# Performance work log

Measured on AMD Instinct MI355X. Metric: run time of the kernel, lower is better.

Reference implementation:

```python
import jax, jax.numpy as jnp
import numpy as np

N = 16777216
BETA = 0.5  # SmoothL1Loss beta

def setup_inputs() -> dict:
    key = jax.random.key(0)
    k1, k2, k3 = jax.random.split(key, 3)
    outs = jax.random.normal(k1, (N,), dtype=jnp.float32)
    labels = jax.random.uniform(k2, (N,), dtype=jnp.float32)
    lens = jax.random.randint(k3, (N,), 1, 1000, dtype=jnp.int64)
    return {"outs": outs, "labels": labels, "lens": lens}

def reference(outs, labels, lens):
    d = outs - labels
    ad = jnp.abs(d)
    # per-element SmoothL1 (beta=0.5); single scalar reduces to 'mean' == value itself
    sl1 = jnp.where(ad < BETA, 0.5 * d * d / BETA, ad - 0.5 * BETA)
    # skip elements whose abs error is within 1/len boundary
    boundary = 1.0 / lens.astype(jnp.float32)
    mask = ad >= boundary
    total = jnp.sum(jnp.where(mask, sl1, 0.0))
    return total.reshape(1)
```

## Files before the change

kernel.cpp:

```cpp
#include <hip/hip_runtime.h>


#define N_TOTAL 16777216
#define NVEC    (N_TOTAL / 4)
#define UNROLL  4
#define BLOCK   256
#define GRID    (NVEC / (BLOCK * UNROLL))

__device__ __forceinline__ float sl1_term(float o, float l, int len) {
    float d  = o - l;
    float ad = fabsf(d);
    float v  = (ad < 0.5f) ? (d * d) : (ad - 0.25f);
    float boundary = 1.0f / (float)len;
    return (ad >= boundary) ? v : 0.0f;
}

__global__ __launch_bounds__(BLOCK) void RegressionLoss_45440753992375_kernel(
        const float* __restrict__ outs,
        const float* __restrict__ labels,
        const int*   __restrict__ lens,
        float* __restrict__ out) {
    const float4* o4 = (const float4*)outs;
    const float4* l4 = (const float4*)labels;
    const int4*   n4 = (const int4*)lens;

    const int base = blockIdx.x * (BLOCK * UNROLL) + threadIdx.x;

    float4 o[UNROLL], l[UNROLL];
    int4   ln[UNROLL];
    #pragma unroll
    for (int u = 0; u < UNROLL; ++u) o[u]  = o4[base + u * BLOCK];
    #pragma unroll
    for (int u = 0; u < UNROLL; ++u) l[u]  = l4[base + u * BLOCK];
    #pragma unroll
    for (int u = 0; u < UNROLL; ++u) ln[u] = n4[base + u * BLOCK];

    float acc = 0.0f;
    #pragma unroll
    for (int u = 0; u < UNROLL; ++u) {
        acc += sl1_term(o[u].x, l[u].x, ln[u].x);
        acc += sl1_term(o[u].y, l[u].y, ln[u].y);
        acc += sl1_term(o[u].z, l[u].z, ln[u].z);
        acc += sl1_term(o[u].w, l[u].w, ln[u].w);
    }

    #pragma unroll
    for (int off = 32; off > 0; off >>= 1)
        acc += __shfl_down(acc, off, 64);

    __shared__ float smem[BLOCK / 64];
    const int lane = threadIdx.x & 63;
    const int wid  = threadIdx.x >> 6;
    if (lane == 0) smem[wid] = acc;
    __syncthreads();
    if (threadIdx.x == 0) {
        float bsum = smem[0] + smem[1] + smem[2] + smem[3];
        atomicAdd(out, bsum);
    }
}

extern "C" void kernel_launch(void* const* d_in, const int* in_sizes, int n_in,
                              void* d_out, int out_size, void* d_ws, size_t ws_size,
                              hipStream_t stream) {
    const float* outs   = (const float*)d_in[0];
    const float* labels = (const float*)d_in[1];
    const int*   lens   = (const int*)d_in[2];
    float* out = (float*)d_out;

    hipMemsetAsync(out, 0, sizeof(float), stream);

    RegressionLoss_45440753992375_kernel<<<GRID, BLOCK, 0, stream>>>(outs, labels, lens, out);
}
```

Measured before the change: 201.0 us.

## Replace unrolled loads with grid-stride loop and one-deep register prefetch

Halves the grid and has each thread iterate over eight float4 chunks, issuing loads for the next chunk before computing the current one. The aim is to overlap memory latency with compute and reduce block count and atomics. It trades the previous four-way batched loads for a single-stage prefetch, which lowers the number of loads in flight per thread.

```diff
diff --git a/kernel.cpp b/kernel.cpp
--- a/kernel.cpp
+++ b/kernel.cpp
@@ -3,9 +3,9 @@
 
 #define N_TOTAL 16777216
 #define NVEC    (N_TOTAL / 4)
-#define UNROLL  4
 #define BLOCK   256
-#define GRID    (NVEC / (BLOCK * UNROLL))
+#define GRID    2048
+#define ITERS   (NVEC / (BLOCK * GRID))
 
 __device__ __forceinline__ float sl1_term(float o, float l, int len) {
     float d  = o - l;
@@ -24,25 +24,31 @@
     const float4* l4 = (const float4*)labels;
     const int4*   n4 = (const int4*)lens;
 
-    const int base = blockIdx.x * (BLOCK * UNROLL) + threadIdx.x;
+    int i = blockIdx.x * (BLOCK * ITERS) + threadIdx.x;
 
-    float4 o[UNROLL], l[UNROLL];
-    int4   ln[UNROLL];
-    #pragma unroll
-    for (int u = 0; u < UNROLL; ++u) o[u]  = o4[base + u * BLOCK];
-    #pragma unroll
-    for (int u = 0; u < UNROLL; ++u) l[u]  = l4[base + u * BLOCK];
-    #pragma unroll
-    for (int u = 0; u < UNROLL; ++u) ln[u] = n4[base + u * BLOCK];
+    float4 o_c = o4[i];
+    float4 l_c = l4[i];
+    int4   n_c = n4[i];
 
     float acc = 0.0f;
     #pragma unroll
-    for (int u = 0; u < UNROLL; ++u) {
-        acc += sl1_term(o[u].x, l[u].x, ln[u].x);
-        acc += sl1_term(o[u].y, l[u].y, ln[u].y);
-        acc += sl1_term(o[u].z, l[u].z, ln[u].z);
-        acc += sl1_term(o[u].w, l[u].w, ln[u].w);
+    for (int it = 0; it < ITERS - 1; ++it) {
+        i += BLOCK;
+        float4 o_n = o4[i];
+        float4 l_n = l4[i];
+        int4   n_n = n4[i];
+
+        acc += sl1_term(o_c.x, l_c.x, n_c.x);
+        acc += sl1_term(o_c.y, l_c.y, n_c.y);
+        acc += sl1_term(o_c.z, l_c.z, n_c.z);
+        acc += sl1_term(o_c.w, l_c.w, n_c.w);
+
+        o_c = o_n; l_c = l_n; n_c = n_n;
     }
+    acc += sl1_term(o_c.x, l_c.x, n_c.x);
+    acc += sl1_term(o_c.y, l_c.y, n_c.y);
+    acc += sl1_term(o_c.z, l_c.z, n_c.z);
+    acc += sl1_term(o_c.w, l_c.w, n_c.w);
 
     #pragma unroll
     for (int off = 32; off > 0; off >>= 1)
```

Result: faster. 195.9 us (-2.5%).
